# Kernel tuning notes

Hardware: AMD Instinct MI355X
Metric: run time of the kernel (lower is better)

Reference implementation:

```python
import jax, jax.numpy as jnp
import numpy as np

SH_BASE = 0.28209479177387814
T_THRESH = 1e-4


def quat_to_rot(q):
    # q: [N,4] (w,x,y,z) -> [N,3,3]
    q = q / jnp.linalg.norm(q, axis=-1, keepdims=True)
    w, x, y, z = q[..., 0], q[..., 1], q[..., 2], q[..., 3]
    return jnp.stack([
        jnp.stack([1 - 2 * (y * y + z * z), 2 * (x * y - w * z), 2 * (x * z + w * y)], -1),
        jnp.stack([2 * (x * y + w * z), 1 - 2 * (x * x + z * z), 2 * (y * z - w * x)], -1),
        jnp.stack([2 * (x * z - w * y), 2 * (y * z + w * x), 1 - 2 * (x * x + y * y)], -1),
    ], -2)


def setup_inputs() -> dict:
    key = jax.random.key(0)
    ks = jax.random.split(key, 6)
    N, H, W = 1024, 256, 256
    u = jax.random.uniform(ks[0], (N, 3))
    z = 2.0 + 6.0 * u[:, 2]  # depths in [2,8], in front of camera
    mean = jnp.stack([(u[:, 0] * 2 - 1) * 0.6 * z, (u[:, 1] * 2 - 1) * 0.6 * z, z], -1)
    qvec = jnp.concatenate([jnp.ones((N, 1)), 0.1 * jax.random.normal(ks[1], (N, 3))], -1)
    svec_b = jnp.log(0.03) + 0.3 * jax.random.normal(ks[2], (N, 3))  # exp-activated scales
    sh = 0.5 * jax.random.normal(ks[3], (N, 3, 9))  # sh_order=3 -> 9 coeffs, only DC used (now_C=1)
    alpha_b = -2.0 + 0.5 * jax.random.normal(ks[4], (N,))  # sigmoid-activated opacity ~0.1
    c2w = jnp.eye(4, dtype=jnp.float32)
    return dict(mean=mean, qvec=qvec, svec_before_activation=svec_b, sh_coeffs=sh,
                alpha_before_activation=alpha_b, c2w=c2w, H=H, W=W)


def reference(mean, qvec, svec_before_activation, sh_coeffs, alpha_before_activation, c2w, H, W):
    fx = float(W); fy = float(W); cx = W / 2.0; cy = H / 2.0
    Rw = c2w[:3, :3].T  # world->camera rotation
    t = c2w[:3, 3]
    p = (mean - t) @ Rw.T  # [N,3] camera-space points
    z = jnp.maximum(p[:, 2], 1e-3)
    # depth sort (front to back), as done by tile_culling_aabb_start_end
    order = jnp.argsort(z)
    p = p[order]; z = z[order]
    qvec = qvec[order]; sb = svec_before_activation[order]
    sh = sh_coeffs[order]; ab = alpha_before_activation[order]
    x, y = p[:, 0], p[:, 1]
    mx, my = x / z, y / z  # projected 2D mean on normalized image plane
    svec = jnp.exp(sb)
    alpha = jax.nn.sigmoid(ab)
    Rq = quat_to_rot(qvec)
    M = Rq * svec[:, None, :]
    cov3d = M @ M.transpose(0, 2, 1)  # [N,3,3]
    cov_cam = jnp.einsum('ij,njk,lk->nil', Rw, cov3d, Rw)
    iz = 1.0 / z; iz2 = iz * iz
    zeros = jnp.zeros_like(iz)
    J = jnp.stack([jnp.stack([iz, zeros, -x * iz2], -1),
                   jnp.stack([zeros, iz, -y * iz2], -1)], -2)  # [N,2,3]
    cov2d = jnp.einsum('nij,njk,nlk->nil', J, cov_cam, J)  # [N,2,2]
    a = cov2d[:, 0, 0] + 1e-8; b = cov2d[:, 0, 1]; c = cov2d[:, 1, 1] + 1e-8
    det = a * c - b * b
    ia, ib, ic = c / det, -b / det, a / det  # inverse 2x2 covariance
    # pixel centers on the normalized image plane
    tlx = -cx / fx; tly = -cy / fy; psx = 1.0 / fx; psy = 1.0 / fy
    px = tlx + (jnp.arange(W, dtype=jnp.float32) + 0.5) * psx  # [W]
    py = tly + (jnp.arange(H, dtype=jnp.float32) + 0.5) * psy  # [H]
    dx = px[None, :] - mx[:, None]  # [N,W]
    dy = py[None, :] - my[:, None]  # [N,H]
    quad = (ia[:, None, None] * (dx * dx)[:, None, :]
            + 2.0 * ib[:, None, None] * dy[:, :, None] * dx[:, None, :]
            + ic[:, None, None] * (dy * dy)[:, :, None])  # [N,H,W]
    G = jnp.exp(-0.5 * quad)
    w = (alpha[:, None, None] * G).reshape(G.shape[0], -1)  # [N,P]
    logw = jnp.log1p(-jnp.clip(w, 0.0, 0.9999))
    cT = jnp.cumsum(logw, axis=0)
    T = jnp.exp(jnp.concatenate([jnp.zeros_like(cT[:1]), cT[:-1]], 0))  # exclusive transmittance
    contrib = jnp.where(T > T_THRESH, w * T, 0.0)  # early termination below T_thresh
    color = jax.nn.sigmoid(SH_BASE * sh[:, :, 0])  # DC SH -> rgb, [N,3]
    out = jnp.einsum('np,nc->pc', contrib, color)
    return out.reshape(H, W, 3)
```

## Files before the change

kernel.cpp:

```cpp
#include <hip/hip_runtime.h>

#define IMG_H 256
#define IMG_W 256
#define NG 1024
#define PSTRIDE 12
#define SH_BASE_F 0.28209479177387814f
#define L2E 1.4426950408889634f
#define LOG2EPS -26.575424759098898f


__global__ __launch_bounds__(256) void preprocess_kernel(
    const float* __restrict__ mean,
    const float* __restrict__ qvec,
    const float* __restrict__ svecb,
    const float* __restrict__ shc,
    const float* __restrict__ alphab,
    const float* __restrict__ c2w,
    unsigned long long* __restrict__ zkey,
    float* __restrict__ tmp,
    int N)
{
    const int i = blockIdx.x * blockDim.x + threadIdx.x;
    if (i >= N) return;

    float C[16];
#pragma unroll
    for (int k = 0; k < 16; ++k) C[k] = c2w[k];
    const float t0 = C[3], t1 = C[7], t2 = C[11];
    const float Rw00 = C[0], Rw01 = C[4], Rw02 = C[8];
    const float Rw10 = C[1], Rw11 = C[5], Rw12 = C[9];
    const float Rw20 = C[2], Rw21 = C[6], Rw22 = C[10];

    const float d0 = mean[3 * i + 0] - t0;
    const float d1 = mean[3 * i + 1] - t1;
    const float d2 = mean[3 * i + 2] - t2;
    const float p0 = Rw00 * d0 + Rw01 * d1 + Rw02 * d2;
    const float p1 = Rw10 * d0 + Rw11 * d1 + Rw12 * d2;
    const float p2 = Rw20 * d0 + Rw21 * d1 + Rw22 * d2;

    const float z  = fmaxf(p2, 0.001f);
    const float iz = 1.0f / z;
    const float mx = p0 * iz;
    const float my = p1 * iz;

    float qw = qvec[4 * i + 0];
    float qx = qvec[4 * i + 1];
    float qy = qvec[4 * i + 2];
    float qz = qvec[4 * i + 3];
    const float qinv = 1.0f / sqrtf(qw * qw + qx * qx + qy * qy + qz * qz);
    qw *= qinv; qx *= qinv; qy *= qinv; qz *= qinv;
    const float R00 = 1.f - 2.f * (qy * qy + qz * qz);
    const float R01 = 2.f * (qx * qy - qw * qz);
    const float R02 = 2.f * (qx * qz + qw * qy);
    const float R10 = 2.f * (qx * qy + qw * qz);
    const float R11 = 1.f - 2.f * (qx * qx + qz * qz);
    const float R12 = 2.f * (qy * qz - qw * qx);
    const float R20 = 2.f * (qx * qz - qw * qy);
    const float R21 = 2.f * (qy * qz + qw * qx);
    const float R22 = 1.f - 2.f * (qx * qx + qy * qy);

    const float s0 = expf(svecb[3 * i + 0]);
    const float s1 = expf(svecb[3 * i + 1]);
    const float s2 = expf(svecb[3 * i + 2]);

    const float M00 = R00 * s0, M01 = R01 * s1, M02 = R02 * s2;
    const float M10 = R10 * s0, M11 = R11 * s1, M12 = R12 * s2;
    const float M20 = R20 * s0, M21 = R21 * s1, M22 = R22 * s2;
    const float V00 = M00 * M00 + M01 * M01 + M02 * M02;
    const float V01 = M00 * M10 + M01 * M11 + M02 * M12;
    const float V02 = M00 * M20 + M01 * M21 + M02 * M22;
    const float V11 = M10 * M10 + M11 * M11 + M12 * M12;
    const float V12 = M10 * M20 + M11 * M21 + M12 * M22;
    const float V22 = M20 * M20 + M21 * M21 + M22 * M22;

    const float A00 = Rw00 * V00 + Rw01 * V01 + Rw02 * V02;
    const float A01 = Rw00 * V01 + Rw01 * V11 + Rw02 * V12;
    const float A02 = Rw00 * V02 + Rw01 * V12 + Rw02 * V22;
    const float A10 = Rw10 * V00 + Rw11 * V01 + Rw12 * V02;
    const float A11 = Rw10 * V01 + Rw11 * V11 + Rw12 * V12;
    const float A12 = Rw10 * V02 + Rw11 * V12 + Rw12 * V22;
    const float A20 = Rw20 * V00 + Rw21 * V01 + Rw22 * V02;
    const float A21 = Rw20 * V01 + Rw21 * V11 + Rw22 * V12;
    const float A22 = Rw20 * V02 + Rw21 * V12 + Rw22 * V22;
    const float CC00 = A00 * Rw00 + A01 * Rw01 + A02 * Rw02;
    const float CC01 = A00 * Rw10 + A01 * Rw11 + A02 * Rw12;
    const float CC02 = A00 * Rw20 + A01 * Rw21 + A02 * Rw22;
    const float CC11 = A10 * Rw10 + A11 * Rw11 + A12 * Rw12;
    const float CC12 = A10 * Rw20 + A11 * Rw21 + A12 * Rw22;
    const float CC22 = A20 * Rw20 + A21 * Rw21 + A22 * Rw22;

    const float iz2 = iz * iz;
    const float j02 = -p0 * iz2, j12 = -p1 * iz2;
    const float T00 = iz * CC00 + j02 * CC02;
    const float T01 = iz * CC01 + j02 * CC12;
    const float T02 = iz * CC02 + j02 * CC22;
    const float T11 = iz * CC11 + j12 * CC12;
    const float T12 = iz * CC12 + j12 * CC22;
    const float c2d00 = T00 * iz + T02 * j02;
    const float c2d01 = T01 * iz + T02 * j12;
    const float c2d11 = T11 * iz + T12 * j12;

    const float a = c2d00 + 1e-8f;
    const float b = c2d01;
    const float c = c2d11 + 1e-8f;
    const float idet = 1.0f / (a * c - b * b);
    const float ia = c * idet, ib = -b * idet, ic = a * idet;

    const float alpha = 1.0f / (1.0f + expf(-alphab[i]));
    const float cr = 1.0f / (1.0f + expf(-SH_BASE_F * shc[27 * i + 0]));
    const float cg = 1.0f / (1.0f + expf(-SH_BASE_F * shc[27 * i + 9]));
    const float cb = 1.0f / (1.0f + expf(-SH_BASE_F * shc[27 * i + 18]));

    zkey[i] = ((unsigned long long)__float_as_uint(z) << 32) | (unsigned)i;

    float4* o4 = (float4*)(tmp + (size_t)i * PSTRIDE);
    o4[0] = make_float4(mx, my, -0.5f * ia * L2E, -ib * L2E);
    o4[1] = make_float4(-0.5f * ic * L2E, log2f(alpha), cr, cg);
    o4[2] = make_float4(cb, 0.f, 0.f, 0.f);
}

__global__ __launch_bounds__(64) void sort_scatter_kernel(
    const unsigned long long* __restrict__ zkey,
    const float* __restrict__ tmp,
    float* __restrict__ pack,
    int N)
{
    __shared__ unsigned long long keys[NG];
    const int tid = threadIdx.x;
#pragma unroll
    for (int k = 0; k < NG / 64; ++k) {
        const int j = k * 64 + tid;
        keys[j] = (j < N) ? zkey[j] : 0xFFFFFFFFFFFFFFFFull;
    }
    __syncthreads();

    const int i = blockIdx.x * 64 + tid;
    if (i >= N) return;
    const unsigned long long ki = keys[i];
    int rank = 0;
#pragma unroll 8
    for (int jb = 0; jb < NG / 2; ++jb) {
        const ulonglong2 kk = ((const ulonglong2*)keys)[jb];
        rank += (kk.x < ki) ? 1 : 0;
        rank += (kk.y < ki) ? 1 : 0;
    }
    const float4* s = (const float4*)(tmp + (size_t)i * PSTRIDE);
    float4* d = (float4*)(pack + (size_t)rank * PSTRIDE);
    d[0] = s[0]; d[1] = s[1]; d[2] = s[2];
}

__global__ __launch_bounds__(256) void render_kernel(
    const float* __restrict__ pack,
    float* __restrict__ out,
    int N)
{
    __shared__ float4 comp[NG][2];
    __shared__ int wcnt[4];

    const int tid = threadIdx.x;
    const int row = blockIdx.x;
    const float py = ((float)row + 0.5f - (float)IMG_H * 0.5f) / (float)IMG_W;
    const int wlane = tid & 63;
    const int wid = tid >> 6;
    const unsigned long long lanemask = (1ull << wlane) - 1ull;

    const float4* pv = (const float4*)pack;

    int cnt = 0;
#pragma unroll
    for (int r = 0; r < 4; ++r) {
        const int n = r * 256 + tid;
        const float4 r0 = pv[n * 3 + 0];
        const float4 r1 = pv[n * 3 + 1];
        const float  bb = pv[n * 3 + 2].x;
        const float dy = py - r0.y;
        const float B  = r0.w * dy;
        const float Cc = fmaf(r1.x * dy, dy, r1.y);
        const float pmax = Cc - (B * B) / (4.0f * r0.z);
        const bool keep = (pmax > LOG2EPS) && (n < N);

        const unsigned long long mask = __ballot(keep);
        if (wlane == 0) wcnt[wid] = __popcll(mask);
        __syncthreads();
        int base = cnt;
#pragma unroll
        for (int w = 0; w < 4; ++w) base += (w < wid) ? wcnt[w] : 0;
        if (keep) {
            const int slot = base + __popcll(mask & lanemask);
            comp[slot][0] = make_float4(r0.x, r0.z, B, Cc);
            comp[slot][1] = make_float4(r1.z, r1.w, bb, 0.f);
        }
        cnt += wcnt[0] + wcnt[1] + wcnt[2] + wcnt[3];
        __syncthreads();
    }

    const int M = cnt;
    const int pad = (32 - (M & 31)) & 31;
    if (tid < pad) {
        comp[M + tid][0] = make_float4(0.f, 0.f, 0.f, -1000.f);
        comp[M + tid][1] = make_float4(0.f, 0.f, 0.f, 0.f);
    }
    __syncthreads();
    const int Mp = M + pad;

    const int jj = tid;
    const float px = ((float)jj + 0.5f - (float)IMG_W * 0.5f) / (float)IMG_W;

    float T = 1.0f;
    float ar = 0.f, ag = 0.f, ab = 0.f;
    for (int mb = 0; mb < Mp; mb += 32) {
#pragma unroll 8
        for (int k = 0; k < 32; ++k) {
            const int m = mb + k;
            const float4 c0 = comp[m][0];
            const float4 c1 = comp[m][1];
            const float dx = px - c0.x;
            const float p  = fmaf(dx, fmaf(c0.y, dx, c0.z), c0.w);
            const float w  = __builtin_amdgcn_exp2f(p);
            const float wT = w * T;
            ar = fmaf(wT, c1.x, ar);
            ag = fmaf(wT, c1.y, ag);
            ab = fmaf(wT, c1.z, ab);
            T = fmaf(-fminf(w, 0.9999f), T, T);
        }
        if (__all(T <= 0.0001f)) break;
    }

    const int o = (row * IMG_W + jj) * 3;
    out[o + 0] = ar;
    out[o + 1] = ag;
    out[o + 2] = ab;
}

extern "C" void kernel_launch(void* const* d_in, const int* in_sizes, int n_in,
                              void* d_out, int out_size, void* d_ws, size_t ws_size,
                              hipStream_t stream)
{
    const float* mean   = (const float*)d_in[0];
    const float* qvec   = (const float*)d_in[1];
    const float* svecb  = (const float*)d_in[2];
    const float* shc    = (const float*)d_in[3];
    const float* alphab = (const float*)d_in[4];
    const float* c2w    = (const float*)d_in[5];

    const int N = in_sizes[0] / 3;

    unsigned long long* zkey = (unsigned long long*)d_ws;
    float* tmp  = (float*)((char*)d_ws + NG * sizeof(unsigned long long));
    float* pack = tmp + (size_t)NG * PSTRIDE;

    preprocess_kernel<<<(N + 255) / 256, 256, 0, stream>>>(
        mean, qvec, svecb, shc, alphab, c2w, zkey, tmp, N);
    sort_scatter_kernel<<<(N + 63) / 64, 64, 0, stream>>>(zkey, tmp, pack, N);
    render_kernel<<<IMG_H, 256, 0, stream>>>(pack, (float*)d_out, N);
}
```

Baseline: 93.21 us.

## Fuse preprocessing, depth sort and rendering into one per-row kernel

Merges the three launches into one render kernel. Each row block recomputes every Gaussian's projection, culls it against the row, then rank-sorts only the surviving Gaussians by depth in shared memory before compositing. This removes two kernel launches and the global round trips through workspace buffers. In exchange each of the 256 blocks repeats the full per-Gaussian preprocessing (exp, sqrt, sigmoid), and it adds a serial rank-count loop over the kept set plus extra shared memory for the keys.

```diff
diff --git a/kernel.cpp b/kernel.cpp
--- a/kernel.cpp
+++ b/kernel.cpp
@@ -3,159 +3,24 @@
 #define IMG_H 256
 #define IMG_W 256
 #define NG 1024
-#define PSTRIDE 12
 #define SH_BASE_F 0.28209479177387814f
 #define L2E 1.4426950408889634f
 #define LOG2EPS -26.575424759098898f
 
-
-__global__ __launch_bounds__(256) void preprocess_kernel(
+__global__ __launch_bounds__(256) void fused_render_kernel(
     const float* __restrict__ mean,
     const float* __restrict__ qvec,
     const float* __restrict__ svecb,
     const float* __restrict__ shc,
     const float* __restrict__ alphab,
     const float* __restrict__ c2w,
-    unsigned long long* __restrict__ zkey,
-    float* __restrict__ tmp,
-    int N)
-{
-    const int i = blockIdx.x * blockDim.x + threadIdx.x;
-    if (i >= N) return;
-
-    float C[16];
-#pragma unroll
-    for (int k = 0; k < 16; ++k) C[k] = c2w[k];
-    const float t0 = C[3], t1 = C[7], t2 = C[11];
-    const float Rw00 = C[0], Rw01 = C[4], Rw02 = C[8];
-    const float Rw10 = C[1], Rw11 = C[5], Rw12 = C[9];
-    const float Rw20 = C[2], Rw21 = C[6], Rw22 = C[10];
-
-    const float d0 = mean[3 * i + 0] - t0;
-    const float d1 = mean[3 * i + 1] - t1;
-    const float d2 = mean[3 * i + 2] - t2;
-    const float p0 = Rw00 * d0 + Rw01 * d1 + Rw02 * d2;
-    const float p1 = Rw10 * d0 + Rw11 * d1 + Rw12 * d2;
-    const float p2 = Rw20 * d0 + Rw21 * d1 + Rw22 * d2;
-
-    const float z  = fmaxf(p2, 0.001f);
-    const float iz = 1.0f / z;
-    const float mx = p0 * iz;
-    const float my = p1 * iz;
-
-    float qw = qvec[4 * i + 0];
-    float qx = qvec[4 * i + 1];
-    float qy = qvec[4 * i + 2];
-    float qz = qvec[4 * i + 3];
-    const float qinv = 1.0f / sqrtf(qw * qw + qx * qx + qy * qy + qz * qz);
-    qw *= qinv; qx *= qinv; qy *= qinv; qz *= qinv;
-    const float R00 = 1.f - 2.f * (qy * qy + qz * qz);
-    const float R01 = 2.f * (qx * qy - qw * qz);
-    const float R02 = 2.f * (qx * qz + qw * qy);
-    const float R10 = 2.f * (qx * qy + qw * qz);
-    const float R11 = 1.f - 2.f * (qx * qx + qz * qz);
-    const float R12 = 2.f * (qy * qz - qw * qx);
-    const float R20 = 2.f * (qx * qz - qw * qy);
-    const float R21 = 2.f * (qy * qz + qw * qx);
-    const float R22 = 1.f - 2.f * (qx * qx + qy * qy);
-
-    const float s0 = expf(svecb[3 * i + 0]);
-    const float s1 = expf(svecb[3 * i + 1]);
-    const float s2 = expf(svecb[3 * i + 2]);
-
-    const float M00 = R00 * s0, M01 = R01 * s1, M02 = R02 * s2;
-    const float M10 = R10 * s0, M11 = R11 * s1, M12 = R12 * s2;
-    const float M20 = R20 * s0, M21 = R21 * s1, M22 = R22 * s2;
-    const float V00 = M00 * M00 + M01 * M01 + M02 * M02;
-    const float V01 = M00 * M10 + M01 * M11 + M02 * M12;
-    const float V02 = M00 * M20 + M01 * M21 + M02 * M22;
-    const float V11 = M10 * M10 + M11 * M11 + M12 * M12;
-    const float V12 = M10 * M20 + M11 * M21 + M12 * M22;
-    const float V22 = M20 * M20 + M21 * M21 + M22 * M22;
-
-    const float A00 = Rw00 * V00 + Rw01 * V01 + Rw02 * V02;
-    const float A01 = Rw00 * V01 + Rw01 * V11 + Rw02 * V12;
-    const float A02 = Rw00 * V02 + Rw01 * V12 + Rw02 * V22;
-    const float A10 = Rw10 * V00 + Rw11 * V01 + Rw12 * V02;
-    const float A11 = Rw10 * V01 + Rw11 * V11 + Rw12 * V12;
-    const float A12 = Rw10 * V02 + Rw11 * V12 + Rw12 * V22;
-    const float A20 = Rw20 * V00 + Rw21 * V01 + Rw22 * V02;
-    const float A21 = Rw20 * V01 + Rw21 * V11 + Rw22 * V12;
-    const float A22 = Rw20 * V02 + Rw21 * V12 + Rw22 * V22;
-    const float CC00 = A00 * Rw00 + A01 * Rw01 + A02 * Rw02;
-    const float CC01 = A00 * Rw10 + A01 * Rw11 + A02 * Rw12;
-    const float CC02 = A00 * Rw20 + A01 * Rw21 + A02 * Rw22;
-    const float CC11 = A10 * Rw10 + A11 * Rw11 + A12 * Rw12;
-    const float CC12 = A10 * Rw20 + A11 * Rw21 + A12 * Rw22;
-    const float CC22 = A20 * Rw20 + A21 * Rw21 + A22 * Rw22;
-
-    const float iz2 = iz * iz;
-    const float j02 = -p0 * iz2, j12 = -p1 * iz2;
-    const float T00 = iz * CC00 + j02 * CC02;
-    const float T01 = iz * CC01 + j02 * CC12;
-    const float T02 = iz * CC02 + j02 * CC22;
-    const float T11 = iz * CC11 + j12 * CC12;
-    const float T12 = iz * CC12 + j12 * CC22;
-    const float c2d00 = T00 * iz + T02 * j02;
-    const float c2d01 = T01 * iz + T02 * j12;
-    const float c2d11 = T11 * iz + T12 * j12;
-
-    const float a = c2d00 + 1e-8f;
-    const float b = c2d01;
-    const float c = c2d11 + 1e-8f;
-    const float idet = 1.0f / (a * c - b * b);
-    const float ia = c * idet, ib = -b * idet, ic = a * idet;
-
-    const float alpha = 1.0f / (1.0f + expf(-alphab[i]));
-    const float cr = 1.0f / (1.0f + expf(-SH_BASE_F * shc[27 * i + 0]));
-    const float cg = 1.0f / (1.0f + expf(-SH_BASE_F * shc[27 * i + 9]));
-    const float cb = 1.0f / (1.0f + expf(-SH_BASE_F * shc[27 * i + 18]));
-
-    zkey[i] = ((unsigned long long)__float_as_uint(z) << 32) | (unsigned)i;
-
-    float4* o4 = (float4*)(tmp + (size_t)i * PSTRIDE);
-    o4[0] = make_float4(mx, my, -0.5f * ia * L2E, -ib * L2E);
-    o4[1] = make_float4(-0.5f * ic * L2E, log2f(alpha), cr, cg);
-    o4[2] = make_float4(cb, 0.f, 0.f, 0.f);
-}
-
-__global__ __launch_bounds__(64) void sort_scatter_kernel(
-    const unsigned long long* __restrict__ zkey,
-    const float* __restrict__ tmp,
-    float* __restrict__ pack,
-    int N)
-{
-    __shared__ unsigned long long keys[NG];
-    const int tid = threadIdx.x;
-#pragma unroll
-    for (int k = 0; k < NG / 64; ++k) {
-        const int j = k * 64 + tid;
-        keys[j] = (j < N) ? zkey[j] : 0xFFFFFFFFFFFFFFFFull;
-    }
-    __syncthreads();
-
-    const int i = blockIdx.x * 64 + tid;
-    if (i >= N) return;
-    const unsigned long long ki = keys[i];
-    int rank = 0;
-#pragma unroll 8
-    for (int jb = 0; jb < NG / 2; ++jb) {
-        const ulonglong2 kk = ((const ulonglong2*)keys)[jb];
-        rank += (kk.x < ki) ? 1 : 0;
-        rank += (kk.y < ki) ? 1 : 0;
-    }
-    const float4* s = (const float4*)(tmp + (size_t)i * PSTRIDE);
-    float4* d = (float4*)(pack + (size_t)rank * PSTRIDE);
-    d[0] = s[0]; d[1] = s[1]; d[2] = s[2];
-}
-
-__global__ __launch_bounds__(256) void render_kernel(
-    const float* __restrict__ pack,
     float* __restrict__ out,
     int N)
 {
     __shared__ float4 comp[NG][2];
+    __shared__ ulonglong2 skey2[NG / 2];
     __shared__ int wcnt[4];
+    unsigned long long* skey = (unsigned long long*)skey2;
 
     const int tid = threadIdx.x;
     const int row = blockIdx.x;
@@ -164,20 +29,112 @@
     const int wid = tid >> 6;
     const unsigned long long lanemask = (1ull << wlane) - 1ull;
 
-    const float4* pv = (const float4*)pack;
+    float C[16];
+#pragma unroll
+    for (int k = 0; k < 16; ++k) C[k] = c2w[k];
+    const float t0 = C[3], t1 = C[7], t2 = C[11];
+    const float Rw00 = C[0], Rw01 = C[4], Rw02 = C[8];
+    const float Rw10 = C[1], Rw11 = C[5], Rw12 = C[9];
+    const float Rw20 = C[2], Rw21 = C[6], Rw22 = C[10];
 
     int cnt = 0;
-#pragma unroll
     for (int r = 0; r < 4; ++r) {
         const int n = r * 256 + tid;
-        const float4 r0 = pv[n * 3 + 0];
-        const float4 r1 = pv[n * 3 + 1];
-        const float  bb = pv[n * 3 + 2].x;
-        const float dy = py - r0.y;
-        const float B  = r0.w * dy;
-        const float Cc = fmaf(r1.x * dy, dy, r1.y);
-        const float pmax = Cc - (B * B) / (4.0f * r0.z);
-        const bool keep = (pmax > LOG2EPS) && (n < N);
+        bool keep = false;
+        float mx = 0.f, qa = 0.f, B = 0.f, Cc = 0.f, cr = 0.f, cg = 0.f, cb = 0.f;
+        unsigned long long zk = 0;
+        if (n < N) {
+            const float d0 = mean[3 * n + 0] - t0;
+            const float d1 = mean[3 * n + 1] - t1;
+            const float d2 = mean[3 * n + 2] - t2;
+            const float p0 = Rw00 * d0 + Rw01 * d1 + Rw02 * d2;
+            const float p1 = Rw10 * d0 + Rw11 * d1 + Rw12 * d2;
+            const float p2 = Rw20 * d0 + Rw21 * d1 + Rw22 * d2;
+
+            const float z  = fmaxf(p2, 0.001f);
+            const float iz = 1.0f / z;
+            mx = p0 * iz;
+            const float my = p1 * iz;
+
+            float qw = qvec[4 * n + 0];
+            float qx = qvec[4 * n + 1];
+            float qy = qvec[4 * n + 2];
+            float qz = qvec[4 * n + 3];
+            const float qinv = 1.0f / sqrtf(qw * qw + qx * qx + qy * qy + qz * qz);
+            qw *= qinv; qx *= qinv; qy *= qinv; qz *= qinv;
+            const float R00 = 1.f - 2.f * (qy * qy + qz * qz);
+            const float R01 = 2.f * (qx * qy - qw * qz);
+            const float R02 = 2.f * (qx * qz + qw * qy);
+            const float R10 = 2.f * (qx * qy + qw * qz);
+            const float R11 = 1.f - 2.f * (qx * qx + qz * qz);
+            const float R12 = 2.f * (qy * qz - qw * qx);
+            const float R20 = 2.f * (qx * qz - qw * qy);
+            const float R21 = 2.f * (qy * qz + qw * qx);
+            const float R22 = 1.f - 2.f * (qx * qx + qy * qy);
+
+            const float s0 = expf(svecb[3 * n + 0]);
+            const float s1 = expf(svecb[3 * n + 1]);
+            const float s2 = expf(svecb[3 * n + 2]);
+
+            const float M00 = R00 * s0, M01 = R01 * s1, M02 = R02 * s2;
+            const float M10 = R10 * s0, M11 = R11 * s1, M12 = R12 * s2;
+            const float M20 = R20 * s0, M21 = R21 * s1, M22 = R22 * s2;
+            const float V00 = M00 * M00 + M01 * M01 + M02 * M02;
+            const float V01 = M00 * M10 + M01 * M11 + M02 * M12;
+            const float V02 = M00 * M20 + M01 * M21 + M02 * M22;
+            const float V11 = M10 * M10 + M11 * M11 + M12 * M12;
+            const float V12 = M10 * M20 + M11 * M21 + M12 * M22;
+            const float V22 = M20 * M20 + M21 * M21 + M22 * M22;
+
+            const float A00 = Rw00 * V00 + Rw01 * V01 + Rw02 * V02;
+            const float A01 = Rw00 * V01 + Rw01 * V11 + Rw02 * V12;
+            const float A02 = Rw00 * V02 + Rw01 * V12 + Rw02 * V22;
+            const float A10 = Rw10 * V00 + Rw11 * V01 + Rw12 * V02;
+            const float A11 = Rw10 * V01 + Rw11 * V11 + Rw12 * V12;
+            const float A12 = Rw10 * V02 + Rw11 * V12 + Rw12 * V22;
+            const float A20 = Rw20 * V00 + Rw21 * V01 + Rw22 * V02;
+            const float A21 = Rw20 * V01 + Rw21 * V11 + Rw22 * V12;
+            const float A22 = Rw20 * V02 + Rw21 * V12 + Rw22 * V22;
+            const float CC00 = A00 * Rw00 + A01 * Rw01 + A02 * Rw02;
+            const float CC01 = A00 * Rw10 + A01 * Rw11 + A02 * Rw12;
+            const float CC02 = A00 * Rw20 + A01 * Rw21 + A02 * Rw22;
+            const float CC11 = A10 * Rw10 + A11 * Rw11 + A12 * Rw12;
+            const float CC12 = A10 * Rw20 + A11 * Rw21 + A12 * Rw22;
+            const float CC22 = A20 * Rw20 + A21 * Rw21 + A22 * Rw22;
+
+            const float iz2 = iz * iz;
+            const float j02 = -p0 * iz2, j12 = -p1 * iz2;
+            const float T00 = iz * CC00 + j02 * CC02;
+            const float T01 = iz * CC01 + j02 * CC12;
+            const float T02 = iz * CC02 + j02 * CC22;
+            const float T11 = iz * CC11 + j12 * CC12;
+            const float T12 = iz * CC12 + j12 * CC22;
+            const float c2d00 = T00 * iz + T02 * j02;
+            const float c2d01 = T01 * iz + T02 * j12;
+            const float c2d11 = T11 * iz + T12 * j12;
+
+            const float a = c2d00 + 1e-8f;
+            const float b = c2d01;
+            const float c = c2d11 + 1e-8f;
+            const float idet = 1.0f / (a * c - b * b);
+            const float ia = c * idet, ib = -b * idet, ic = a * idet;
+
+            qa = -0.5f * ia * L2E;
+            const float qb = -ib * L2E;
+            const float qc = -0.5f * ic * L2E;
+            const float alpha = 1.0f / (1.0f + expf(-alphab[n]));
+            const float la = log2f(alpha);
+            cr = 1.0f / (1.0f + expf(-SH_BASE_F * shc[27 * n + 0]));
+            cg = 1.0f / (1.0f + expf(-SH_BASE_F * shc[27 * n + 9]));
+            cb = 1.0f / (1.0f + expf(-SH_BASE_F * shc[27 * n + 18]));
+
+            const float dy = py - my;
+            B  = qb * dy;
+            Cc = fmaf(qc * dy, dy, la);
+            const float pmax = Cc - (B * B) / (4.0f * qa);
+            keep = (pmax > LOG2EPS);
+            zk = ((unsigned long long)__float_as_uint(z) << 32) | (unsigned)n;
+        }
 
         const unsigned long long mask = __ballot(keep);
         if (wlane == 0) wcnt[wid] = __popcll(mask);
@@ -187,8 +144,9 @@
         for (int w = 0; w < 4; ++w) base += (w < wid) ? wcnt[w] : 0;
         if (keep) {
             const int slot = base + __popcll(mask & lanemask);
-            comp[slot][0] = make_float4(r0.x, r0.z, B, Cc);
-            comp[slot][1] = make_float4(r1.z, r1.w, bb, 0.f);
+            comp[slot][0] = make_float4(mx, qa, B, Cc);
+            comp[slot][1] = make_float4(cr, cg, cb, 0.f);
+            skey[slot] = zk;
         }
         cnt += wcnt[0] + wcnt[1] + wcnt[2] + wcnt[3];
         __syncthreads();
@@ -199,13 +157,41 @@
     if (tid < pad) {
         comp[M + tid][0] = make_float4(0.f, 0.f, 0.f, -1000.f);
         comp[M + tid][1] = make_float4(0.f, 0.f, 0.f, 0.f);
+        skey[M + tid] = 0xFFFFFFFF00000000ull | (unsigned)(M + tid);
     }
     __syncthreads();
     const int Mp = M + pad;
 
-    const int jj = tid;
-    const float px = ((float)jj + 0.5f - (float)IMG_W * 0.5f) / (float)IMG_W;
-
+    float4 sr0[4], sr1[4];
+    int srk[4];
+#pragma unroll
+    for (int q = 0; q < 4; ++q) {
+        const int s = q * 256 + tid;
+        if (s < Mp) {
+            const unsigned long long k = skey[s];
+            int rank = 0;
+            for (int jb = 0; jb < (Mp >> 1); ++jb) {
+                const ulonglong2 kk = skey2[jb];
+                rank += (kk.x < k) ? 1 : 0;
+                rank += (kk.y < k) ? 1 : 0;
+            }
+            sr0[q] = comp[s][0];
+            sr1[q] = comp[s][1];
+            srk[q] = rank;
+        }
+    }
+    __syncthreads();
+#pragma unroll
+    for (int q = 0; q < 4; ++q) {
+        const int s = q * 256 + tid;
+        if (s < Mp) {
+            comp[srk[q]][0] = sr0[q];
+            comp[srk[q]][1] = sr1[q];
+        }
+    }
+    __syncthreads();
+
+    const float px = ((float)tid + 0.5f - (float)IMG_W * 0.5f) / (float)IMG_W;
     float T = 1.0f;
     float ar = 0.f, ag = 0.f, ab = 0.f;
     for (int mb = 0; mb < Mp; mb += 32) {
@@ -226,7 +212,7 @@
         if (__all(T <= 0.0001f)) break;
     }
 
-    const int o = (row * IMG_W + jj) * 3;
+    const int o = (row * IMG_W + tid) * 3;
     out[o + 0] = ar;
     out[o + 1] = ag;
     out[o + 2] = ab;
@@ -245,12 +231,6 @@
 
     const int N = in_sizes[0] / 3;
 
-    unsigned long long* zkey = (unsigned long long*)d_ws;
-    float* tmp  = (float*)((char*)d_ws + NG * sizeof(unsigned long long));
-    float* pack = tmp + (size_t)NG * PSTRIDE;
-
-    preprocess_kernel<<<(N + 255) / 256, 256, 0, stream>>>(
-        mean, qvec, svecb, shc, alphab, c2w, zkey, tmp, N);
-    sort_scatter_kernel<<<(N + 63) / 64, 64, 0, stream>>>(zkey, tmp, pack, N);
-    render_kernel<<<IMG_H, 256, 0, stream>>>(pack, (float*)d_out, N);
+    fused_render_kernel<<<IMG_H, 256, 0, stream>>>(
+        mean, qvec, svecb, shc, alphab, c2w, (float*)d_out, N);
 }
```

Measured after the change: 78.71 us. 1.18x faster.
